# Performance work log

Hardware: AMD Instinct MI355X
Metric: run time of the kernel (lower is better)

The kernel has to match this reference:

```python
import jax, jax.numpy as jnp
import numpy as np

DIM = 384
HEADS = 6
DIM_HEAD = 64
INNER = HEADS * DIM_HEAD  # 384


def setup_inputs() -> dict:
    key = jax.random.key(0)
    ks = jax.random.split(key, 6)
    s = 0.02
    return {
        "x_q": jax.random.normal(ks[0], (8, 4096, DIM), dtype=jnp.float32),
        "x_kv": jax.random.normal(ks[1], (8, 4096, DIM), dtype=jnp.float32),
        "Wq": jax.random.normal(ks[2], (DIM, INNER), dtype=jnp.float32) * s,
        "Wkv": jax.random.normal(ks[3], (DIM, 2 * INNER), dtype=jnp.float32) * s,
        "Wout": jax.random.normal(ks[4], (INNER, DIM), dtype=jnp.float32) * s,
        "bout": jax.random.normal(ks[5], (DIM,), dtype=jnp.float32) * s,
    }


def _split_heads(t, b, n):
    # [b, n, h*d] -> [b, h, n, d]
    return t.reshape(b, n, HEADS, DIM_HEAD).transpose(0, 2, 1, 3)


def reference(x_q, x_kv, Wq, Wkv, Wout, bout):
    b, nq, _ = x_q.shape
    nkv = x_kv.shape[1]
    q = x_q @ Wq                      # [b, nq, inner]
    kv_proj = x_kv @ Wkv              # [b, nkv, 2*inner]
    k, v = jnp.split(kv_proj, 2, axis=-1)
    q = _split_heads(q, b, nq)        # [b, h, nq, d]
    k = _split_heads(k, b, nkv)       # [b, h, nkv, d]
    v = _split_heads(v, b, nkv)       # [b, h, nkv, d]
    q = jax.nn.elu(q) + 1.0
    k = jax.nn.elu(k) + 1.0
    kv = jnp.einsum('bhnd,bhnm->bhdm', k, v)             # [b, h, d, d]
    z = 1.0 / (jnp.einsum('bhnd,bhd->bhn', q, k.sum(axis=2)) + 1e-6)
    out = jnp.einsum('bhnd,bhdm->bhnm', q, kv) * z[..., None]  # [b, h, nq, d]
    out = out.transpose(0, 2, 1, 3).reshape(b, nq, INNER)
    return out @ Wout + bout
```

## Files before the change

kernel.cpp:

```cpp
#include <hip/hip_runtime.h>
#include <math.h>

#define BATCH 8
#define SEQ 4096
#define DIMSZ 384
#define HEADS 6
#define DH 64
#define MTOT (BATCH * SEQ)
#define KD 384

typedef short short8 __attribute__((ext_vector_type(8)));
typedef float floatx4 __attribute__((ext_vector_type(4)));
typedef unsigned short ushort4v __attribute__((ext_vector_type(4)));
typedef unsigned short ushort8v __attribute__((ext_vector_type(8)));

__device__ __forceinline__ float elu1(float x) { return x > 0.f ? x + 1.f : __expf(x); }

__device__ __forceinline__ unsigned short f2b(float f) {
    unsigned int u = __float_as_uint(f);
    u = (u + 0x7fffu + ((u >> 16) & 1u)) >> 16;
    return (unsigned short)u;
}
__device__ __forceinline__ float b2f(unsigned short u) {
    return __uint_as_float(((unsigned int)u) << 16);
}

__device__ __forceinline__ void gl16(const void* g, void* l) {
    __builtin_amdgcn_global_load_lds((const __attribute__((address_space(1))) unsigned int*)g,
                                     (__attribute__((address_space(3))) unsigned int*)l, 16, 0, 0);
}

__global__ __launch_bounds__(256) void conv_bf16(const float* __restrict__ src,
                                                 unsigned short* __restrict__ dst) {
    size_t i = ((size_t)blockIdx.x * 256 + threadIdx.x) * 8;
    float4 a = *(const float4*)&src[i];
    float4 b = *(const float4*)&src[i + 4];
    ushort8v o;
    o[0] = f2b(a.x); o[1] = f2b(a.y); o[2] = f2b(a.z); o[3] = f2b(a.w);
    o[4] = f2b(b.x); o[5] = f2b(b.y); o[6] = f2b(b.z); o[7] = f2b(b.w);
    *(ushort8v*)&dst[i] = o;
}

__global__ __launch_bounds__(256) void conv_wt3(const float* __restrict__ Wq,
                                                const float* __restrict__ Wkv,
                                                const float* __restrict__ Wout,
                                                unsigned short* __restrict__ WqT,
                                                unsigned short* __restrict__ WkvT,
                                                unsigned short* __restrict__ WoutT) {
    __shared__ float tile[32][33];
    int bx = blockIdx.x;
    const float* W;
    unsigned short* WT;
    int N;
    if (bx < 12) { W = Wq; WT = WqT; N = DIMSZ; }
    else if (bx < 36) { W = Wkv; WT = WkvT; N = 2 * DIMSZ; bx -= 12; }
    else { W = Wout; WT = WoutT; N = DIMSZ; bx -= 36; }
    const int n0 = bx * 32, k0 = blockIdx.y * 32;
    const int tx = threadIdx.x & 31, ty = threadIdx.x >> 5;
#pragma unroll
    for (int i = 0; i < 32; i += 8) tile[ty + i][tx] = W[(size_t)(k0 + ty + i) * N + n0 + tx];
    __syncthreads();
#pragma unroll
    for (int i = 0; i < 32; i += 8)
        WT[(size_t)(n0 + ty + i) * KD + k0 + tx] = f2b(tile[tx][ty + i]);
}

template <int EPI, int NC>
__global__ __launch_bounds__(256) void gemm_bt(const unsigned short* __restrict__ A,
                                               const unsigned short* __restrict__ BT,
                                               void* __restrict__ Cout,
                                               const float* __restrict__ bias) {
    __shared__ __align__(16) unsigned short buf[17408];
    unsigned short* As = buf;
    unsigned short* Bs = buf + 8192;
    const int tid = threadIdx.x;
    const int lane = tid & 63, wave = tid >> 6;
    const int l15 = lane & 15, qd = lane >> 4;
    constexpr int NXT = NC / 128;
    const int fid = blockIdx.x;
    const int xcd = fid & 7;
    const int s = fid >> 3;
    const int row0 = (xcd * 32 + s / NXT) * 128;
    const int col0 = (s % NXT) * 128;
    const int wm = (wave & 1) * 64, wn = (wave >> 1) * 64;

    const unsigned short* Ab = A + (size_t)row0 * KD;
    const unsigned short* Bb = BT + (size_t)col0 * KD;
    const int srow = tid >> 3;
    const int scol = (((tid & 7) ^ (srow & 7)) * 8);

    floatx4 zero = {0.f, 0.f, 0.f, 0.f};
    floatx4 acc[4][4];
#pragma unroll
    for (int i = 0; i < 4; ++i)
#pragma unroll
        for (int j = 0; j < 4; ++j) acc[i][j] = zero;

    const int sw = l15 & 7;
    for (int kk = 0; kk < KD; kk += 64) {
        __syncthreads();
#pragma unroll
        for (int i = 0; i < 4; ++i)
            gl16(Ab + (size_t)(i * 32 + srow) * KD + kk + scol, As + i * 2048 + wave * 512);
#pragma unroll
        for (int i = 0; i < 4; ++i)
            gl16(Bb + (size_t)(i * 32 + srow) * KD + kk + scol, Bs + i * 2048 + wave * 512);
        __syncthreads();
#pragma unroll
        for (int t = 0; t < 2; ++t) {
            const int chnk = ((t * 4 + qd) ^ sw) * 8;
            short8 af[4], bfr[4];
#pragma unroll
            for (int mi = 0; mi < 4; ++mi)
                af[mi] = *(const short8*)&As[(wm + mi * 16 + l15) * 64 + chnk];
#pragma unroll
            for (int ni = 0; ni < 4; ++ni)
                bfr[ni] = *(const short8*)&Bs[(wn + ni * 16 + l15) * 64 + chnk];
#pragma unroll
            for (int mi = 0; mi < 4; ++mi)
#pragma unroll
                for (int ni = 0; ni < 4; ++ni)
                    acc[mi][ni] = __builtin_amdgcn_mfma_f32_16x16x32_bf16(af[mi], bfr[ni],
                                                                          acc[mi][ni], 0, 0, 0);
        }
    }

    if (EPI == 2) {
        float* C = (float*)Cout;
#pragma unroll
        for (int mi = 0; mi < 4; ++mi)
#pragma unroll
            for (int ni = 0; ni < 4; ++ni) {
                const int rbase = row0 + wm + mi * 16 + qd * 4;
                const int col = col0 + wn + ni * 16 + l15;
                const float bsv = bias[col];
#pragma unroll
                for (int r = 0; r < 4; ++r)
                    __builtin_nontemporal_store(acc[mi][ni][r] + bsv,
                                                &C[(size_t)(rbase + r) * NC + col]);
            }
    } else if (EPI == 0) {
        unsigned short* C = (unsigned short*)Cout;
#pragma unroll
        for (int mi = 0; mi < 4; ++mi)
#pragma unroll
            for (int ni = 0; ni < 4; ++ni) {
                const int rbase = row0 + wm + mi * 16 + qd * 4;
                const int col = col0 + wn + ni * 16 + l15;
#pragma unroll
                for (int r = 0; r < 4; ++r)
                    C[(size_t)(rbase + r) * NC + col] = f2b(elu1(acc[mi][ni][r]));
            }
    } else {
        __syncthreads();
#pragma unroll
        for (int mi = 0; mi < 4; ++mi)
#pragma unroll
            for (int ni = 0; ni < 4; ++ni) {
                const int rb = wm + mi * 16 + qd * 4;
                const int cl = wn + ni * 16 + l15;
                const bool act = (col0 + cl) < DIMSZ;
                ushort4v o;
#pragma unroll
                for (int r = 0; r < 4; ++r) {
                    float v = acc[mi][ni][r];
                    o[r] = f2b(act ? elu1(v) : v);
                }
                *(ushort4v*)&buf[cl * 136 + rb] = o;
            }
        __syncthreads();
        unsigned short* CT = (unsigned short*)Cout;
        const int c0 = tid >> 4, rr = (tid & 15) * 8;
#pragma unroll
        for (int p = 0; p < 8; ++p) {
            const int col = c0 + p * 16;
            ushort8v v = *(const ushort8v*)&buf[col * 136 + rr];
            __builtin_nontemporal_store(v,
                                        (ushort8v*)&CT[(size_t)(col0 + col) * MTOT + row0 + rr]);
        }
    }
}

__global__ __launch_bounds__(256) void kv_state_mfma(const unsigned short* __restrict__ kvpT,
                                                     float* __restrict__ pkv,
                                                     float* __restrict__ pks) {
    __shared__ float kvLDS[4096];
    __shared__ float ksLDS[64];
    const int bx = blockIdx.x;
    const int bh = bx >> 4, ch = bx & 15;
    const int b = bh / HEADS, h = bh % HEADS;
    const int tid = threadIdx.x;
    const int lane = tid & 63, wave = tid >> 6;
    const int l15 = lane & 15, qd = lane >> 4;
    const size_t nbase = (size_t)b * SEQ + ch * 256 + wave * 64;
    const unsigned short* kbase = kvpT + (size_t)(h * 64) * MTOT + nbase;
    const unsigned short* vbase = kvpT + (size_t)(DIMSZ + h * 64) * MTOT + nbase;

    floatx4 zero = {0.f, 0.f, 0.f, 0.f};
    floatx4 acc[4][4];
#pragma unroll
    for (int i = 0; i < 4; ++i)
#pragma unroll
        for (int j = 0; j < 4; ++j) acc[i][j] = zero;
    float ksa[4] = {};

#pragma unroll
    for (int t = 0; t < 2; ++t) {
        short8 af[4], bfr[4];
#pragma unroll
        for (int mi = 0; mi < 4; ++mi)
            af[mi] = *(const short8*)&kbase[(size_t)(mi * 16 + l15) * MTOT + t * 32 + qd * 8];
#pragma unroll
        for (int ni = 0; ni < 4; ++ni)
            bfr[ni] = *(const short8*)&vbase[(size_t)(ni * 16 + l15) * MTOT + t * 32 + qd * 8];
#pragma unroll
        for (int mi = 0; mi < 4; ++mi) {
#pragma unroll
            for (int j = 0; j < 8; ++j) ksa[mi] += b2f((unsigned short)af[mi][j]);
#pragma unroll
            for (int ni = 0; ni < 4; ++ni)
                acc[mi][ni] =
                    __builtin_amdgcn_mfma_f32_16x16x32_bf16(af[mi], bfr[ni], acc[mi][ni], 0, 0, 0);
        }
    }
#pragma unroll
    for (int mi = 0; mi < 4; ++mi) {
        float v = ksa[mi];
        v += __shfl_xor(v, 16);
        v += __shfl_xor(v, 32);
        ksa[mi] = v;
    }
    for (int w = 0; w < 4; ++w) {
        if (wave == w) {
#pragma unroll
            for (int mi = 0; mi < 4; ++mi)
#pragma unroll
                for (int ni = 0; ni < 4; ++ni)
#pragma unroll
                    for (int r = 0; r < 4; ++r) {
                        const int idx = (mi * 16 + qd * 4 + r) * 64 + ni * 16 + l15;
                        if (w == 0) kvLDS[idx] = acc[mi][ni][r];
                        else kvLDS[idx] += acc[mi][ni][r];
                    }
            if (lane < 16) {
#pragma unroll
                for (int mi = 0; mi < 4; ++mi) {
                    if (w == 0) ksLDS[mi * 16 + lane] = ksa[mi];
                    else ksLDS[mi * 16 + lane] += ksa[mi];
                }
            }
        }
        __syncthreads();
    }
    const int base = tid * 16;
#pragma unroll
    for (int i = 0; i < 16; i += 4)
        *(float4*)&pkv[(size_t)bx * 4096 + base + i] = *(float4*)&kvLDS[base + i];
    if (tid < 64) pks[bx * 64 + tid] = ksLDS[tid];
}

__global__ __launch_bounds__(256) void kv_reduce(const float* __restrict__ pkv,
                                                 const float* __restrict__ pks,
                                                 float* __restrict__ kv_g,
                                                 float* __restrict__ ksum_g) {
    const int bh = blockIdx.x;
    const int tid = threadIdx.x;
    for (int i0 = tid * 4; i0 < 4096; i0 += 1024) {
        float4 s = {0.f, 0.f, 0.f, 0.f};
#pragma unroll
        for (int c = 0; c < 16; ++c) {
            float4 p = *(const float4*)&pkv[(size_t)(bh * 16 + c) * 4096 + i0];
            s.x += p.x; s.y += p.y; s.z += p.z; s.w += p.w;
        }
        *(float4*)&kv_g[(size_t)bh * 4096 + i0] = s;
    }
    if (tid < 64) {
        float s = 0.f;
#pragma unroll
        for (int c = 0; c < 16; ++c) s += pks[(bh * 16 + c) * 64 + tid];
        ksum_g[bh * 64 + tid] = s;
    }
}

__global__ __launch_bounds__(256) void attn_mfma(const unsigned short* __restrict__ q,
                                                 const float* __restrict__ kv_g,
                                                 const float* __restrict__ ksum_g,
                                                 unsigned short* __restrict__ attn) {
    __shared__ __align__(16) unsigned short kvbs[64 * 72];
    __shared__ float ksh[64];
    __shared__ float zsh[256];
    const int bx = blockIdx.x;
    const int bh = bx >> 4;
    const int rt = bx & 15;
    const int b = bh / HEADS, h = bh % HEADS;
    const int tid = threadIdx.x;
    const int lane = tid & 63, wave = tid >> 6;
    const int l15 = lane & 15, qd = lane >> 4;
#pragma unroll
    for (int i = 0; i < 16; ++i) {
        int e = i * 256 + tid;
        int d = e >> 6, m = e & 63;
        kvbs[m * 72 + d] = f2b(kv_g[(size_t)bh * 4096 + e]);
    }
    if (tid < 64) ksh[tid] = ksum_g[bh * 64 + tid];
    __syncthreads();
    const size_t rowbase = (size_t)b * SEQ + rt * 256;
    floatx4 zero = {0.f, 0.f, 0.f, 0.f};
    floatx4 acc[4][4];
#pragma unroll
    for (int i = 0; i < 4; ++i)
#pragma unroll
        for (int j = 0; j < 4; ++j) acc[i][j] = zero;
    float zp[4] = {};
#pragma unroll
    for (int ks = 0; ks < 2; ++ks) {
        short8 bfr[4];
#pragma unroll
        for (int ni = 0; ni < 4; ++ni)
            bfr[ni] = *(const short8*)&kvbs[(ni * 16 + l15) * 72 + ks * 32 + qd * 8];
#pragma unroll
        for (int mi = 0; mi < 4; ++mi) {
            short8 af = *(const short8*)&q[(rowbase + wave * 64 + mi * 16 + l15) * KD + h * 64 +
                                           ks * 32 + qd * 8];
#pragma unroll
            for (int j = 0; j < 8; ++j)
                zp[mi] += b2f((unsigned short)af[j]) * ksh[ks * 32 + qd * 8 + j];
#pragma unroll
            for (int ni = 0; ni < 4; ++ni)
                acc[mi][ni] =
                    __builtin_amdgcn_mfma_f32_16x16x32_bf16(af, bfr[ni], acc[mi][ni], 0, 0, 0);
        }
    }
#pragma unroll
    for (int mi = 0; mi < 4; ++mi) {
        float v = zp[mi];
        v += __shfl_xor(v, 16);
        v += __shfl_xor(v, 32);
        if (lane < 16) zsh[wave * 64 + mi * 16 + lane] = 1.f / (v + 1e-6f);
    }
    __syncthreads();
#pragma unroll
    for (int mi = 0; mi < 4; ++mi) {
#pragma unroll
        for (int ni = 0; ni < 4; ++ni) {
            const int rl = wave * 64 + mi * 16 + qd * 4;
            const int col = h * 64 + ni * 16 + l15;
#pragma unroll
            for (int r = 0; r < 4; ++r) {
                float v = acc[mi][ni][r] * zsh[rl + r];
                attn[(rowbase + rl + r) * KD + col] = f2b(v);
            }
        }
    }
}

extern "C" void kernel_launch(void* const* d_in, const int* in_sizes, int n_in,
                              void* d_out, int out_size, void* d_ws, size_t ws_size,
                              hipStream_t stream) {
    const float* x_q = (const float*)d_in[0];
    const float* x_kv = (const float*)d_in[1];
    const float* Wq = (const float*)d_in[2];
    const float* Wkv = (const float*)d_in[3];
    const float* Wout = (const float*)d_in[4];
    const float* bout = (const float*)d_in[5];
    float* out = (float*)d_out;

    char* ws = (char*)d_ws;
    unsigned short* x_bf = (unsigned short*)(ws + 0);
    unsigned short* kvpT = (unsigned short*)(ws + 25165824);
    unsigned short* q_bf = (unsigned short*)(ws + 50331648);
    unsigned short* WqT = (unsigned short*)(ws + 75497472);
    unsigned short* WkvT = (unsigned short*)(ws + 75792384);
    unsigned short* WoutT = (unsigned short*)(ws + 76382208);
    float* kv = (float*)(ws + 76677120);
    float* ksum = (float*)(ws + 77463552);
    float* pkv = (float*)(ws + 77475840);
    float* pks = (float*)(ws + 90058752);

    dim3 blk(256);
    conv_wt3<<<dim3(48, 12), blk, 0, stream>>>(Wq, Wkv, Wout, WqT, WkvT, WoutT);
    conv_bf16<<<dim3(6144), blk, 0, stream>>>(x_kv, x_bf);
    gemm_bt<3, 768><<<dim3(1536), blk, 0, stream>>>(x_bf, WkvT, kvpT, nullptr);
    kv_state_mfma<<<dim3(768), blk, 0, stream>>>(kvpT, pkv, pks);
    kv_reduce<<<dim3(48), blk, 0, stream>>>(pkv, pks, kv, ksum);
    conv_bf16<<<dim3(6144), blk, 0, stream>>>(x_q, x_bf);
    gemm_bt<0, 384><<<dim3(768), blk, 0, stream>>>(x_bf, WqT, q_bf, nullptr);
    attn_mfma<<<dim3(768), blk, 0, stream>>>(q_bf, kv, ksum, q_bf);
    gemm_bt<2, 384><<<dim3(768), blk, 0, stream>>>(q_bf, WoutT, out, bout);
}
```

Baseline: 265.6 us.

## Fuse K/V projection with kv-state and Q projection with attention apply

The KV projection GEMM now tiles per head, taking the 64 K columns and the 64 V columns of one head for each 128-row tile. It computes the k^T v partial state and the k-sum in its epilogue, so the transposed kvp intermediate is never written and kv_state is no longer a separate kernel. The Q projection GEMM is fused with the attention apply: it computes q^T tiles, applies ELU, computes the normaliser, and multiplies by the per-head kv state held in LDS. This removes the round trip of q through global memory. The two input conversions are merged into one launch, and partial sums grow to 32 per head, which adds reduce work and more LDS per block.

New measurement: 273.7 us. 3.0% more time.

```diff
diff --git a/kernel.cpp b/kernel.cpp
--- a/kernel.cpp
+++ b/kernel.cpp
@@ -30,9 +30,16 @@
                                      (__attribute__((address_space(3))) unsigned int*)l, 16, 0, 0);
 }
 
-__global__ __launch_bounds__(256) void conv_bf16(const float* __restrict__ src,
-                                                 unsigned short* __restrict__ dst) {
-    size_t i = ((size_t)blockIdx.x * 256 + threadIdx.x) * 8;
+__global__ __launch_bounds__(256) void conv_x2(const float* __restrict__ xq,
+                                               const float* __restrict__ xkv,
+                                               unsigned short* __restrict__ dq,
+                                               unsigned short* __restrict__ dkv) {
+    int bx = blockIdx.x;
+    const float* src;
+    unsigned short* dst;
+    if (bx < 6144) { src = xkv; dst = dkv; }
+    else { src = xq; dst = dq; bx -= 6144; }
+    size_t i = ((size_t)bx * 256 + threadIdx.x) * 8;
     float4 a = *(const float4*)&src[i];
     float4 b = *(const float4*)&src[i + 4];
     ushort8v o;
@@ -65,27 +72,28 @@
         WT[(size_t)(n0 + ty + i) * KD + k0 + tx] = f2b(tile[tx][ty + i]);
 }
 
-template <int EPI, int NC>
-__global__ __launch_bounds__(256) void gemm_bt(const unsigned short* __restrict__ A,
-                                               const unsigned short* __restrict__ BT,
-                                               void* __restrict__ Cout,
-                                               const float* __restrict__ bias) {
+__global__ __launch_bounds__(256) void gemm_kv(const unsigned short* __restrict__ A,
+                                               const unsigned short* __restrict__ WkvT,
+                                               float* __restrict__ pkv,
+                                               float* __restrict__ pks) {
     __shared__ __align__(16) unsigned short buf[17408];
+    __shared__ float ksLDS[128];
     unsigned short* As = buf;
     unsigned short* Bs = buf + 8192;
     const int tid = threadIdx.x;
     const int lane = tid & 63, wave = tid >> 6;
     const int l15 = lane & 15, qd = lane >> 4;
-    constexpr int NXT = NC / 128;
     const int fid = blockIdx.x;
     const int xcd = fid & 7;
     const int s = fid >> 3;
-    const int row0 = (xcd * 32 + s / NXT) * 128;
-    const int col0 = (s % NXT) * 128;
+    const int h = s % HEADS;
+    const int rtl = s / HEADS;
+    const int row0 = (xcd * 32 + rtl) * 128;
+    const int pidx = (xcd * HEADS + h) * 32 + rtl;
     const int wm = (wave & 1) * 64, wn = (wave >> 1) * 64;
 
     const unsigned short* Ab = A + (size_t)row0 * KD;
-    const unsigned short* Bb = BT + (size_t)col0 * KD;
+    const unsigned short* Bb = WkvT + (size_t)(h * DH) * KD;
     const int srow = tid >> 3;
     const int scol = (((tid & 7) ^ (srow & 7)) * 8);
 
@@ -104,7 +112,8 @@
             gl16(Ab + (size_t)(i * 32 + srow) * KD + kk + scol, As + i * 2048 + wave * 512);
 #pragma unroll
         for (int i = 0; i < 4; ++i)
-            gl16(Bb + (size_t)(i * 32 + srow) * KD + kk + scol, Bs + i * 2048 + wave * 512);
+            gl16(Bb + (size_t)(i * 32 + srow + (i >= 2 ? 320 : 0)) * KD + kk + scol,
+                 Bs + i * 2048 + wave * 512);
         __syncthreads();
 #pragma unroll
         for (int t = 0; t < 2; ++t) {
@@ -125,138 +134,63 @@
         }
     }
 
-    if (EPI == 2) {
-        float* C = (float*)Cout;
+    float ksp[4] = {};
+    if (wn == 0) {
 #pragma unroll
         for (int mi = 0; mi < 4; ++mi)
 #pragma unroll
-            for (int ni = 0; ni < 4; ++ni) {
-                const int rbase = row0 + wm + mi * 16 + qd * 4;
-                const int col = col0 + wn + ni * 16 + l15;
-                const float bsv = bias[col];
-#pragma unroll
-                for (int r = 0; r < 4; ++r)
-                    __builtin_nontemporal_store(acc[mi][ni][r] + bsv,
-                                                &C[(size_t)(rbase + r) * NC + col]);
+            for (int ni = 0; ni < 4; ++ni)
+#pragma unroll
+                for (int r = 0; r < 4; ++r) ksp[ni] += elu1(acc[mi][ni][r]);
+#pragma unroll
+        for (int ni = 0; ni < 4; ++ni) {
+            float v = ksp[ni];
+            v += __shfl_xor(v, 16);
+            v += __shfl_xor(v, 32);
+            ksp[ni] = v;
+        }
+    }
+    __syncthreads();
+    if (wn == 0 && lane < 16) {
+#pragma unroll
+        for (int ni = 0; ni < 4; ++ni) ksLDS[wave * 64 + ni * 16 + lane] = ksp[ni];
+    }
+#pragma unroll
+    for (int mi = 0; mi < 4; ++mi)
+#pragma unroll
+        for (int ni = 0; ni < 4; ++ni) {
+            const int rb = wm + mi * 16 + qd * 4;
+            const int cl = wn + ni * 16 + l15;
+            ushort4v o;
+#pragma unroll
+            for (int r = 0; r < 4; ++r) {
+                float v = acc[mi][ni][r];
+                o[r] = f2b(cl < 64 ? elu1(v) : v);
             }
-    } else if (EPI == 0) {
-        unsigned short* C = (unsigned short*)Cout;
-#pragma unroll
-        for (int mi = 0; mi < 4; ++mi)
-#pragma unroll
-            for (int ni = 0; ni < 4; ++ni) {
-                const int rbase = row0 + wm + mi * 16 + qd * 4;
-                const int col = col0 + wn + ni * 16 + l15;
-#pragma unroll
-                for (int r = 0; r < 4; ++r)
-                    C[(size_t)(rbase + r) * NC + col] = f2b(elu1(acc[mi][ni][r]));
-            }
-    } else {
-        __syncthreads();
-#pragma unroll
-        for (int mi = 0; mi < 4; ++mi)
-#pragma unroll
-            for (int ni = 0; ni < 4; ++ni) {
-                const int rb = wm + mi * 16 + qd * 4;
-                const int cl = wn + ni * 16 + l15;
-                const bool act = (col0 + cl) < DIMSZ;
-                ushort4v o;
-#pragma unroll
-                for (int r = 0; r < 4; ++r) {
-                    float v = acc[mi][ni][r];
-                    o[r] = f2b(act ? elu1(v) : v);
-                }
-                *(ushort4v*)&buf[cl * 136 + rb] = o;
-            }
-        __syncthreads();
-        unsigned short* CT = (unsigned short*)Cout;
-        const int c0 = tid >> 4, rr = (tid & 15) * 8;
-#pragma unroll
-        for (int p = 0; p < 8; ++p) {
-            const int col = c0 + p * 16;
-            ushort8v v = *(const ushort8v*)&buf[col * 136 + rr];
-            __builtin_nontemporal_store(v,
-                                        (ushort8v*)&CT[(size_t)(col0 + col) * MTOT + row0 + rr]);
-        }
-    }
-}
-
-__global__ __launch_bounds__(256) void kv_state_mfma(const unsigned short* __restrict__ kvpT,
-                                                     float* __restrict__ pkv,
-                                                     float* __restrict__ pks) {
-    __shared__ float kvLDS[4096];
-    __shared__ float ksLDS[64];
-    const int bx = blockIdx.x;
-    const int bh = bx >> 4, ch = bx & 15;
-    const int b = bh / HEADS, h = bh % HEADS;
-    const int tid = threadIdx.x;
-    const int lane = tid & 63, wave = tid >> 6;
-    const int l15 = lane & 15, qd = lane >> 4;
-    const size_t nbase = (size_t)b * SEQ + ch * 256 + wave * 64;
-    const unsigned short* kbase = kvpT + (size_t)(h * 64) * MTOT + nbase;
-    const unsigned short* vbase = kvpT + (size_t)(DIMSZ + h * 64) * MTOT + nbase;
-
-    floatx4 zero = {0.f, 0.f, 0.f, 0.f};
-    floatx4 acc[4][4];
-#pragma unroll
-    for (int i = 0; i < 4; ++i)
-#pragma unroll
-        for (int j = 0; j < 4; ++j) acc[i][j] = zero;
-    float ksa[4] = {};
-
-#pragma unroll
-    for (int t = 0; t < 2; ++t) {
-        short8 af[4], bfr[4];
-#pragma unroll
-        for (int mi = 0; mi < 4; ++mi)
-            af[mi] = *(const short8*)&kbase[(size_t)(mi * 16 + l15) * MTOT + t * 32 + qd * 8];
-#pragma unroll
-        for (int ni = 0; ni < 4; ++ni)
-            bfr[ni] = *(const short8*)&vbase[(size_t)(ni * 16 + l15) * MTOT + t * 32 + qd * 8];
-#pragma unroll
-        for (int mi = 0; mi < 4; ++mi) {
-#pragma unroll
-            for (int j = 0; j < 8; ++j) ksa[mi] += b2f((unsigned short)af[mi][j]);
-#pragma unroll
-            for (int ni = 0; ni < 4; ++ni)
-                acc[mi][ni] =
-                    __builtin_amdgcn_mfma_f32_16x16x32_bf16(af[mi], bfr[ni], acc[mi][ni], 0, 0, 0);
-        }
-    }
-#pragma unroll
-    for (int mi = 0; mi < 4; ++mi) {
-        float v = ksa[mi];
-        v += __shfl_xor(v, 16);
-        v += __shfl_xor(v, 32);
-        ksa[mi] = v;
-    }
-    for (int w = 0; w < 4; ++w) {
-        if (wave == w) {
-#pragma unroll
-            for (int mi = 0; mi < 4; ++mi)
-#pragma unroll
-                for (int ni = 0; ni < 4; ++ni)
-#pragma unroll
-                    for (int r = 0; r < 4; ++r) {
-                        const int idx = (mi * 16 + qd * 4 + r) * 64 + ni * 16 + l15;
-                        if (w == 0) kvLDS[idx] = acc[mi][ni][r];
-                        else kvLDS[idx] += acc[mi][ni][r];
-                    }
-            if (lane < 16) {
-#pragma unroll
-                for (int mi = 0; mi < 4; ++mi) {
-                    if (w == 0) ksLDS[mi * 16 + lane] = ksa[mi];
-                    else ksLDS[mi * 16 + lane] += ksa[mi];
-                }
-            }
-        }
-        __syncthreads();
-    }
-    const int base = tid * 16;
-#pragma unroll
-    for (int i = 0; i < 16; i += 4)
-        *(float4*)&pkv[(size_t)bx * 4096 + base + i] = *(float4*)&kvLDS[base + i];
-    if (tid < 64) pks[bx * 64 + tid] = ksLDS[tid];
+            *(ushort4v*)&buf[cl * 136 + rb] = o;
+        }
+    __syncthreads();
+    floatx4 kva[4];
+#pragma unroll
+    for (int j = 0; j < 4; ++j) kva[j] = zero;
+#pragma unroll
+    for (int nk = 0; nk < 4; ++nk) {
+        short8 afk = *(const short8*)&buf[(wave * 16 + l15) * 136 + nk * 32 + qd * 8];
+#pragma unroll
+        for (int nj = 0; nj < 4; ++nj) {
+            short8 bfv = *(const short8*)&buf[(64 + nj * 16 + l15) * 136 + nk * 32 + qd * 8];
+            kva[nj] = __builtin_amdgcn_mfma_f32_16x16x32_bf16(afk, bfv, kva[nj], 0, 0, 0);
+        }
+    }
+    float* P = pkv + (size_t)pidx * 4096;
+#pragma unroll
+    for (int nj = 0; nj < 4; ++nj)
+#pragma unroll
+        for (int r = 0; r < 4; ++r)
+            __builtin_nontemporal_store(kva[nj][r],
+                                        &P[(wave * 16 + qd * 4 + r) * 64 + nj * 16 + l15]);
+    if (tid < 64)
+        __builtin_nontemporal_store(ksLDS[tid] + ksLDS[64 + tid], &pks[pidx * 64 + tid]);
 }
 
 __global__ __launch_bounds__(256) void kv_reduce(const float* __restrict__ pkv,
@@ -266,92 +200,237 @@
     const int bh = blockIdx.x;
     const int tid = threadIdx.x;
     for (int i0 = tid * 4; i0 < 4096; i0 += 1024) {
-        float4 s = {0.f, 0.f, 0.f, 0.f};
-#pragma unroll
-        for (int c = 0; c < 16; ++c) {
-            float4 p = *(const float4*)&pkv[(size_t)(bh * 16 + c) * 4096 + i0];
-            s.x += p.x; s.y += p.y; s.z += p.z; s.w += p.w;
-        }
-        *(float4*)&kv_g[(size_t)bh * 4096 + i0] = s;
+        float4 sum = {0.f, 0.f, 0.f, 0.f};
+#pragma unroll
+        for (int c = 0; c < 32; ++c) {
+            float4 p = *(const float4*)&pkv[(size_t)(bh * 32 + c) * 4096 + i0];
+            sum.x += p.x; sum.y += p.y; sum.z += p.z; sum.w += p.w;
+        }
+        *(float4*)&kv_g[(size_t)bh * 4096 + i0] = sum;
     }
     if (tid < 64) {
-        float s = 0.f;
-#pragma unroll
-        for (int c = 0; c < 16; ++c) s += pks[(bh * 16 + c) * 64 + tid];
-        ksum_g[bh * 64 + tid] = s;
-    }
-}
-
-__global__ __launch_bounds__(256) void attn_mfma(const unsigned short* __restrict__ q,
-                                                 const float* __restrict__ kv_g,
-                                                 const float* __restrict__ ksum_g,
-                                                 unsigned short* __restrict__ attn) {
-    __shared__ __align__(16) unsigned short kvbs[64 * 72];
-    __shared__ float ksh[64];
+        float sum = 0.f;
+#pragma unroll
+        for (int c = 0; c < 32; ++c) sum += pks[(bh * 32 + c) * 64 + tid];
+        ksum_g[bh * 64 + tid] = sum;
+    }
+}
+
+__global__ __launch_bounds__(256) void gemm_q_attn(const unsigned short* __restrict__ A,
+                                                   const unsigned short* __restrict__ WqT,
+                                                   const float* __restrict__ kv_g,
+                                                   const float* __restrict__ ksum_g,
+                                                   unsigned short* __restrict__ attn) {
+    __shared__ __align__(16) unsigned short buf[17408];
+    __shared__ __align__(16) unsigned short kvb[9216];
+    __shared__ float ksh[128];
     __shared__ float zsh[256];
-    const int bx = blockIdx.x;
-    const int bh = bx >> 4;
-    const int rt = bx & 15;
-    const int b = bh / HEADS, h = bh % HEADS;
+    unsigned short* As = buf;
+    unsigned short* Bs = buf + 8192;
     const int tid = threadIdx.x;
     const int lane = tid & 63, wave = tid >> 6;
     const int l15 = lane & 15, qd = lane >> 4;
-#pragma unroll
-    for (int i = 0; i < 16; ++i) {
-        int e = i * 256 + tid;
-        int d = e >> 6, m = e & 63;
-        kvbs[m * 72 + d] = f2b(kv_g[(size_t)bh * 4096 + e]);
-    }
-    if (tid < 64) ksh[tid] = ksum_g[bh * 64 + tid];
-    __syncthreads();
-    const size_t rowbase = (size_t)b * SEQ + rt * 256;
+    const int fid = blockIdx.x;
+    const int xcd = fid & 7;
+    const int s = fid >> 3;
+    const int ct = s % 3;
+    const int rtl = s / 3;
+    const int row0 = (xcd * 32 + rtl) * 128;
+    const int col0 = ct * 128;
+    const int bh0 = xcd * HEADS + ct * 2;
+    const int wd = (wave & 1) * 64, wn2 = (wave >> 1) * 64;
+
+#pragma unroll
+    for (int i = 0; i < 32; ++i) {
+        const int e = i * 256 + tid;
+        const int hh2 = e >> 12, rr = e & 4095;
+        kvb[hh2 * 4608 + (rr & 63) * 72 + (rr >> 6)] = f2b(kv_g[(size_t)(bh0 + hh2) * 4096 + rr]);
+    }
+    if (tid < 128) ksh[tid] = ksum_g[bh0 * 64 + tid];
+
+    const unsigned short* Ab = A + (size_t)row0 * KD;
+    const unsigned short* Bb = WqT + (size_t)col0 * KD;
+    const int srow = tid >> 3;
+    const int scol = (((tid & 7) ^ (srow & 7)) * 8);
+
     floatx4 zero = {0.f, 0.f, 0.f, 0.f};
     floatx4 acc[4][4];
 #pragma unroll
     for (int i = 0; i < 4; ++i)
 #pragma unroll
         for (int j = 0; j < 4; ++j) acc[i][j] = zero;
+
+    const int sw = l15 & 7;
+    for (int kk = 0; kk < KD; kk += 64) {
+        __syncthreads();
+#pragma unroll
+        for (int i = 0; i < 4; ++i)
+            gl16(Ab + (size_t)(i * 32 + srow) * KD + kk + scol, As + i * 2048 + wave * 512);
+#pragma unroll
+        for (int i = 0; i < 4; ++i)
+            gl16(Bb + (size_t)(i * 32 + srow) * KD + kk + scol, Bs + i * 2048 + wave * 512);
+        __syncthreads();
+#pragma unroll
+        for (int t = 0; t < 2; ++t) {
+            const int chnk = ((t * 4 + qd) ^ sw) * 8;
+            short8 wf[4], xf[4];
+#pragma unroll
+            for (int di = 0; di < 4; ++di)
+                wf[di] = *(const short8*)&Bs[(wd + di * 16 + l15) * 64 + chnk];
+#pragma unroll
+            for (int nj = 0; nj < 4; ++nj)
+                xf[nj] = *(const short8*)&As[(wn2 + nj * 16 + l15) * 64 + chnk];
+#pragma unroll
+            for (int di = 0; di < 4; ++di)
+#pragma unroll
+                for (int nj = 0; nj < 4; ++nj)
+                    acc[di][nj] = __builtin_amdgcn_mfma_f32_16x16x32_bf16(wf[di], xf[nj],
+                                                                          acc[di][nj], 0, 0, 0);
+        }
+    }
+
     float zp[4] = {};
 #pragma unroll
-    for (int ks = 0; ks < 2; ++ks) {
-        short8 bfr[4];
-#pragma unroll
-        for (int ni = 0; ni < 4; ++ni)
-            bfr[ni] = *(const short8*)&kvbs[(ni * 16 + l15) * 72 + ks * 32 + qd * 8];
-#pragma unroll
-        for (int mi = 0; mi < 4; ++mi) {
-            short8 af = *(const short8*)&q[(rowbase + wave * 64 + mi * 16 + l15) * KD + h * 64 +
-                                           ks * 32 + qd * 8];
-#pragma unroll
-            for (int j = 0; j < 8; ++j)
-                zp[mi] += b2f((unsigned short)af[j]) * ksh[ks * 32 + qd * 8 + j];
-#pragma unroll
-            for (int ni = 0; ni < 4; ++ni)
-                acc[mi][ni] =
-                    __builtin_amdgcn_mfma_f32_16x16x32_bf16(af, bfr[ni], acc[mi][ni], 0, 0, 0);
-        }
-    }
-#pragma unroll
-    for (int mi = 0; mi < 4; ++mi) {
-        float v = zp[mi];
+    for (int di = 0; di < 4; ++di)
+#pragma unroll
+        for (int r = 0; r < 4; ++r) {
+            const float ks = ksh[wd + di * 16 + qd * 4 + r];
+#pragma unroll
+            for (int nj = 0; nj < 4; ++nj) {
+                const float q = elu1(acc[di][nj][r]);
+                acc[di][nj][r] = q;
+                zp[nj] += q * ks;
+            }
+        }
+#pragma unroll
+    for (int nj = 0; nj < 4; ++nj) {
+        float v = zp[nj];
         v += __shfl_xor(v, 16);
         v += __shfl_xor(v, 32);
-        if (lane < 16) zsh[wave * 64 + mi * 16 + lane] = 1.f / (v + 1e-6f);
+        zp[nj] = 1.f / (v + 1e-6f);
     }
     __syncthreads();
-#pragma unroll
-    for (int mi = 0; mi < 4; ++mi) {
+    if (lane < 16) {
+#pragma unroll
+        for (int nj = 0; nj < 4; ++nj) zsh[(wave & 1) * 128 + wn2 + nj * 16 + lane] = zp[nj];
+    }
+#pragma unroll
+    for (int di = 0; di < 4; ++di)
+#pragma unroll
+        for (int nj = 0; nj < 4; ++nj) {
+            const int rb = wd + di * 16 + qd * 4;
+            const int cl = wn2 + nj * 16 + l15;
+            ushort4v o;
+#pragma unroll
+            for (int r = 0; r < 4; ++r) o[r] = f2b(acc[di][nj][r]);
+            *(ushort4v*)&buf[cl * 136 + rb] = o;
+        }
+    __syncthreads();
+    const int hh = wave & 1;
+    floatx4 acc2[4][4];
+#pragma unroll
+    for (int i = 0; i < 4; ++i)
+#pragma unroll
+        for (int j = 0; j < 4; ++j) acc2[i][j] = zero;
+#pragma unroll
+    for (int t = 0; t < 2; ++t) {
+        short8 bf2[4];
+#pragma unroll
+        for (int bj = 0; bj < 4; ++bj)
+            bf2[bj] = *(const short8*)&kvb[hh * 4608 + (bj * 16 + l15) * 72 + t * 32 + qd * 8];
+#pragma unroll
+        for (int ai = 0; ai < 4; ++ai) {
+            short8 af =
+                *(const short8*)&buf[(wn2 + ai * 16 + l15) * 136 + hh * 64 + t * 32 + qd * 8];
+#pragma unroll
+            for (int bj = 0; bj < 4; ++bj)
+                acc2[ai][bj] =
+                    __builtin_amdgcn_mfma_f32_16x16x32_bf16(af, bf2[bj], acc2[ai][bj], 0, 0, 0);
+        }
+    }
+#pragma unroll
+    for (int ai = 0; ai < 4; ++ai)
+#pragma unroll
+        for (int bj = 0; bj < 4; ++bj) {
+            const int colg = col0 + hh * 64 + bj * 16 + l15;
+#pragma unroll
+            for (int r = 0; r < 4; ++r) {
+                const int nl = wn2 + ai * 16 + qd * 4 + r;
+                const float v = acc2[ai][bj][r] * zsh[hh * 128 + nl];
+                attn[(size_t)(row0 + nl) * KD + colg] = f2b(v);
+            }
+        }
+}
+
+__global__ __launch_bounds__(256) void gemm_out(const unsigned short* __restrict__ A,
+                                                const unsigned short* __restrict__ BT,
+                                                float* __restrict__ C,
+                                                const float* __restrict__ bias) {
+    __shared__ __align__(16) unsigned short buf[17408];
+    unsigned short* As = buf;
+    unsigned short* Bs = buf + 8192;
+    const int tid = threadIdx.x;
+    const int lane = tid & 63, wave = tid >> 6;
+    const int l15 = lane & 15, qd = lane >> 4;
+    const int fid = blockIdx.x;
+    const int xcd = fid & 7;
+    const int s = fid >> 3;
+    const int row0 = (xcd * 32 + s / 3) * 128;
+    const int col0 = (s % 3) * 128;
+    const int wm = (wave & 1) * 64, wn = (wave >> 1) * 64;
+
+    const unsigned short* Ab = A + (size_t)row0 * KD;
+    const unsigned short* Bb = BT + (size_t)col0 * KD;
+    const int srow = tid >> 3;
+    const int scol = (((tid & 7) ^ (srow & 7)) * 8);
+
+    floatx4 zero = {0.f, 0.f, 0.f, 0.f};
+    floatx4 acc[4][4];
+#pragma unroll
+    for (int i = 0; i < 4; ++i)
+#pragma unroll
+        for (int j = 0; j < 4; ++j) acc[i][j] = zero;
+
+    const int sw = l15 & 7;
+    for (int kk = 0; kk < KD; kk += 64) {
+        __syncthreads();
+#pragma unroll
+        for (int i = 0; i < 4; ++i)
+            gl16(Ab + (size_t)(i * 32 + srow) * KD + kk + scol, As + i * 2048 + wave * 512);
+#pragma unroll
+        for (int i = 0; i < 4; ++i)
+            gl16(Bb + (size_t)(i * 32 + srow) * KD + kk + scol, Bs + i * 2048 + wave * 512);
+        __syncthreads();
+#pragma unroll
+        for (int t = 0; t < 2; ++t) {
+            const int chnk = ((t * 4 + qd) ^ sw) * 8;
+            short8 af[4], bfr[4];
+#pragma unroll
+            for (int mi = 0; mi < 4; ++mi)
+                af[mi] = *(const short8*)&As[(wm + mi * 16 + l15) * 64 + chnk];
+#pragma unroll
+            for (int ni = 0; ni < 4; ++ni)
+                bfr[ni] = *(const short8*)&Bs[(wn + ni * 16 + l15) * 64 + chnk];
+#pragma unroll
+            for (int mi = 0; mi < 4; ++mi)
+#pragma unroll
+                for (int ni = 0; ni < 4; ++ni)
+                    acc[mi][ni] = __builtin_amdgcn_mfma_f32_16x16x32_bf16(af[mi], bfr[ni],
+                                                                          acc[mi][ni], 0, 0, 0);
+        }
+    }
+#pragma unroll
+    for (int mi = 0; mi < 4; ++mi)
 #pragma unroll
         for (int ni = 0; ni < 4; ++ni) {
-            const int rl = wave * 64 + mi * 16 + qd * 4;
-            const int col = h * 64 + ni * 16 + l15;
-#pragma unroll
-            for (int r = 0; r < 4; ++r) {
-                float v = acc[mi][ni][r] * zsh[rl + r];
-                attn[(rowbase + rl + r) * KD + col] = f2b(v);
-            }
-        }
-    }
+            const int rbase = row0 + wm + mi * 16 + qd * 4;
+            const int col = col0 + wn + ni * 16 + l15;
+            const float bsv = bias[col];
+#pragma unroll
+            for (int r = 0; r < 4; ++r)
+                __builtin_nontemporal_store(acc[mi][ni][r] + bsv,
+                                            &C[(size_t)(rbase + r) * DIMSZ + col]);
+        }
 }
 
 extern "C" void kernel_launch(void* const* d_in, const int* in_sizes, int n_in,
@@ -366,25 +445,22 @@
     float* out = (float*)d_out;
 
     char* ws = (char*)d_ws;
-    unsigned short* x_bf = (unsigned short*)(ws + 0);
-    unsigned short* kvpT = (unsigned short*)(ws + 25165824);
-    unsigned short* q_bf = (unsigned short*)(ws + 50331648);
+    unsigned short* xq_bf = (unsigned short*)(ws + 0);
+    unsigned short* xkv_bf = (unsigned short*)(ws + 25165824);
+    float* pkv = (float*)(ws + 50331648);
+    unsigned short* attn_bf = (unsigned short*)(ws + 50331648);
     unsigned short* WqT = (unsigned short*)(ws + 75497472);
     unsigned short* WkvT = (unsigned short*)(ws + 75792384);
     unsigned short* WoutT = (unsigned short*)(ws + 76382208);
     float* kv = (float*)(ws + 76677120);
     float* ksum = (float*)(ws + 77463552);
-    float* pkv = (float*)(ws + 77475840);
-    float* pks = (float*)(ws + 90058752);
+    float* pks = (float*)(ws + 77475840);
 
     dim3 blk(256);
     conv_wt3<<<dim3(48, 12), blk, 0, stream>>>(Wq, Wkv, Wout, WqT, WkvT, WoutT);
-    conv_bf16<<<dim3(6144), blk, 0, stream>>>(x_kv, x_bf);
-    gemm_bt<3, 768><<<dim3(1536), blk, 0, stream>>>(x_bf, WkvT, kvpT, nullptr);
-    kv_state_mfma<<<dim3(768), blk, 0, stream>>>(kvpT, pkv, pks);
+    conv_x2<<<dim3(12288), blk, 0, stream>>>(x_q, x_kv, xq_bf, xkv_bf);
+    gemm_kv<<<dim3(1536), blk, 0, stream>>>(xkv_bf, WkvT, pkv, pks);
     kv_reduce<<<dim3(48), blk, 0, stream>>>(pkv, pks, kv, ksum);
-    conv_bf16<<<dim3(6144), blk, 0, stream>>>(x_q, x_bf);
-    gemm_bt<0, 384><<<dim3(768), blk, 0, stream>>>(x_bf, WqT, q_bf, nullptr);
-    attn_mfma<<<dim3(768), blk, 0, stream>>>(q_bf, kv, ksum, q_bf);
-    gemm_bt<2, 384><<<dim3(768), blk, 0, stream>>>(q_bf, WoutT, out, bout);
-}
+    gemm_q_attn<<<dim3(768), blk, 0, stream>>>(xq_bf, WqT, kv, ksum, attn_bf);
+    gemm_out<<<dim3(768), blk, 0, stream>>>(attn_bf, WoutT, out, bout);
+}
```
